# Kernel optimization log

Hardware: AMD Instinct MI355X
Metric: run time of the kernel (lower is better)

Reference implementation:

```python
import jax, jax.numpy as jnp
import numpy as np

B, H, L, N = 16, 128, 4096, 64
DT_MIN, DT_MAX = 0.001, 0.1


def _make_dplr_hippo(n):
    # NPLR HiPPO -> DPLR diagonalization (numpy, init-time only)
    p0 = np.sqrt(1 + 2 * np.arange(n))
    A = p0[:, None] * p0[None, :]
    A = -(np.tril(A) - np.diag(np.arange(n)))
    p = np.sqrt(np.arange(n) + 0.5)
    b = np.sqrt(2 * np.arange(n) + 1.0)
    S = A + p[:, None] * p[None, :]
    Lam_re = np.mean(np.diagonal(S)) * np.ones(n)
    Lam_im, V = np.linalg.eigh(S * -1j)
    p = V.conj().T @ p
    b = V.conj().T @ b
    return Lam_re + 1j * Lam_im, p, b


def setup_inputs() -> dict:
    key = jax.random.key(0)
    k1, k2, k3 = jax.random.split(key, 3)
    Lam, p, b = _make_dplr_hippo(N)
    tile = lambda a: jnp.tile(jnp.asarray(a, jnp.float32)[None], (H, 1))
    Lambda_re = tile(Lam.real)
    Lambda_im = tile(Lam.imag)
    P_ri = jnp.tile(jnp.stack([jnp.asarray(p.real, jnp.float32), jnp.asarray(p.imag, jnp.float32)], -1)[None], (H, 1, 1))
    B_ri = jnp.tile(jnp.stack([jnp.asarray(b.real, jnp.float32), jnp.asarray(b.imag, jnp.float32)], -1)[None], (H, 1, 1))
    C = (0.5 ** 0.5) * jax.random.normal(k1, (H, N, 2), jnp.float32)
    log_step = jax.random.uniform(k2, (H,)) * (np.log(DT_MAX) - np.log(DT_MIN)) + np.log(DT_MIN)
    D = jnp.ones((H,), jnp.float32)
    u = jax.random.normal(k3, (B, H, L), jnp.float32)
    return {"u": u, "Lambda_re": Lambda_re, "Lambda_im": Lambda_im, "P_ri": P_ri,
            "B_ri": B_ri, "C": C, "log_step": log_step.astype(jnp.float32), "D": D}


def reference(u, Lambda_re, Lambda_im, P_ri, B_ri, C, log_step, D):
    Lseq = u.shape[-1]
    # setup(): Lambda = clip(Lambda_re, max=-1e-4) + i*Lambda_im ; C complex ; step = exp(log_step)
    Lam = jnp.minimum(Lambda_re, -1e-4) + 1j * Lambda_im            # [H,N]
    P = P_ri[..., 0] + 1j * P_ri[..., 1]                             # [H,N]
    Bm = B_ri[..., 0] + 1j * B_ri[..., 1]                            # [H,N]
    Cc = C[..., 0] + 1j * C[..., 1]                                  # [H,N]
    step = jnp.exp(log_step)                                         # [H]
    # kernel_DPLR at the roots of unity
    Omega = jnp.exp(-2j * jnp.pi * (jnp.arange(Lseq) / Lseq))        # [L]
    g = (2.0 / step)[:, None] * ((1.0 - Omega) / (1.0 + Omega))[None, :]  # [H,L]
    c = 2.0 / (1.0 + Omega)                                          # [L]
    den = 1.0 / (g[:, :, None] - Lam[:, None, :])                    # [H,L,N] resolvent
    # four Cauchy dot products, batched: v stacked on last axis
    Vmat = jnp.stack([Cc.conj() * Bm, Cc.conj() * P, P.conj() * Bm, P.conj() * P], axis=-1)  # [H,N,4]
    Ks = jnp.einsum('hln,hnk->hlk', den, Vmat)                       # [H,L,4]
    k00, k01, k10, k11 = Ks[..., 0], Ks[..., 1], Ks[..., 2], Ks[..., 3]
    atRoots = c[None, :] * (k00 - k01 * (1.0 / (1.0 + k11)) * k10)   # [H,L]
    K = jnp.fft.ifft(atRoots, Lseq, axis=-1).real                    # [H,L] SSM kernel
    # causal FFT convolution: pad both to 2L
    ud = jnp.fft.rfft(jnp.pad(u, ((0, 0), (0, 0), (0, Lseq))), axis=-1)   # [B,H,L+1]
    Kd = jnp.fft.rfft(jnp.pad(K, ((0, 0), (0, Lseq))), axis=-1)           # [H,L+1]
    y = jnp.fft.irfft(ud * Kd[None], axis=-1)[..., :Lseq]            # [B,H,L]
    return y + D[None, :, None] * u
```

## Files before the change

### kernel.cpp

```cpp
#include <hip/hip_runtime.h>
#include <hip/hip_bf16.h>


#define PI_F 3.14159265358979323846f

__device__ __forceinline__ float2 cmulf(float2 a, float2 b) {
  return make_float2(a.x * b.x - a.y * b.y, a.x * b.y + a.y * b.x);
}
__device__ __forceinline__ void cmul_set(float2& v, float wr, float wi) {
  v = make_float2(v.x * wr - v.y * wi, v.x * wi + v.y * wr);
}
__device__ __forceinline__ int ad(int k) { return k + (k >> 4); }

template <int SIGN>
__device__ __forceinline__ void bfly4(float2& a, float2& b, float2& c,
                                      float2& d) {
  float t0x = a.x + c.x, t0y = a.y + c.y;
  float t1x = a.x - c.x, t1y = a.y - c.y;
  float t2x = b.x + d.x, t2y = b.y + d.y;
  float t3x = b.x - d.x, t3y = b.y - d.y;
  a = make_float2(t0x + t2x, t0y + t2y);
  c = make_float2(t0x - t2x, t0y - t2y);
  if (SIGN < 0) {
    b = make_float2(t1x + t3y, t1y - t3x);
    d = make_float2(t1x - t3y, t1y + t3x);
  } else {
    b = make_float2(t1x - t3y, t1y + t3x);
    d = make_float2(t1x + t3y, t1y - t3x);
  }
}

template <int SIGN>
__device__ __forceinline__ void fft16(float2 v[16]) {
  const float sg = (float)SIGN;
  const float C1 = 0.92387953251128674f;
  const float S1 = 0.38268343236508978f;
  const float R2 = 0.70710678118654752f;
  bfly4<SIGN>(v[0], v[4], v[8], v[12]);
  bfly4<SIGN>(v[1], v[5], v[9], v[13]);
  bfly4<SIGN>(v[2], v[6], v[10], v[14]);
  bfly4<SIGN>(v[3], v[7], v[11], v[15]);
  cmul_set(v[5], C1, sg * S1);
  cmul_set(v[6], R2, sg * R2);
  cmul_set(v[7], S1, sg * C1);
  cmul_set(v[9], R2, sg * R2);
  v[10] = make_float2(-sg * v[10].y, sg * v[10].x);
  cmul_set(v[11], -R2, sg * R2);
  cmul_set(v[13], S1, sg * C1);
  cmul_set(v[14], -R2, sg * R2);
  cmul_set(v[15], -C1, -sg * S1);
  float2 w[16];
#pragma unroll
  for (int g = 0; g < 4; ++g) {
    float2 x0 = v[4 * g], x1 = v[4 * g + 1], x2 = v[4 * g + 2],
           x3 = v[4 * g + 3];
    bfly4<SIGN>(x0, x1, x2, x3);
    w[g] = x0; w[g + 4] = x1; w[g + 8] = x2; w[g + 12] = x3;
  }
#pragma unroll
  for (int i = 0; i < 16; ++i) v[i] = w[i];
}

__device__ __forceinline__ void tw_apply(float2 v[16], float ang) {
  float sn, cn;
  __sincosf(ang, &sn, &cn);
  float2 w1 = make_float2(cn, sn), cw = w1;
#pragma unroll
  for (int g = 1; g < 16; ++g) {
    v[g] = cmulf(v[g], cw);
    if (g < 15) cw = cmulf(cw, w1);
  }
}

template <int SIGN>
__device__ void fft4096_regs(float2 v[16], float2* lds, int tid) {
  const int a = tid & 15, g2 = tid >> 4;
  fft16<SIGN>(v);
  tw_apply(v, (float)SIGN * (2.0f * PI_F / 4096.0f) * (float)tid);
  __syncthreads();
#pragma unroll
  for (int g = 0; g < 16; ++g) lds[tid * 17 + g] = v[g];
  __syncthreads();
#pragma unroll
  for (int b = 0; b < 16; ++b) v[b] = lds[a * 17 + b * 272 + g2];
  fft16<SIGN>(v);
  tw_apply(v, (float)SIGN * (2.0f * PI_F / 256.0f) * (float)a);
  __syncthreads();
#pragma unroll
  for (int b = 0; b < 16; ++b) lds[g2 * 17 + b * 273 + a] = v[b];
  __syncthreads();
#pragma unroll
  for (int a2 = 0; a2 < 16; ++a2) v[a2] = lds[g2 * 17 + a * 273 + a2];
  fft16<SIGN>(v);
}

template <int SIGN>
__device__ void fft4096_scr2nat(float2 v[16], float2* lds, int tid) {
  const int a = tid & 15, g2 = tid >> 4;
  fft16<SIGN>(v);
  __syncthreads();
#pragma unroll
  for (int r = 0; r < 16; ++r) lds[g2 * 17 + a * 273 + r] = v[r];
  __syncthreads();
#pragma unroll
  for (int b = 0; b < 16; ++b) v[b] = lds[g2 * 17 + b * 273 + a];
  tw_apply(v, (float)SIGN * (2.0f * PI_F / 256.0f) * (float)a);
  fft16<SIGN>(v);
  __syncthreads();
#pragma unroll
  for (int r = 0; r < 16; ++r) lds[272 * r + 17 * a + g2] = v[r];
  __syncthreads();
#pragma unroll
  for (int g = 0; g < 16; ++g) v[g] = lds[tid * 17 + g];
  tw_apply(v, (float)SIGN * (2.0f * PI_F / 4096.0f) * (float)tid);
  fft16<SIGN>(v);
}

__global__ __launch_bounds__(256) void k_cauchy(
    const float* __restrict__ Lre, const float* __restrict__ Lim,
    const float* __restrict__ Pri, const float* __restrict__ Bri,
    const float* __restrict__ Cri, const float* __restrict__ lstep,
    float2* __restrict__ atR) {
  __shared__ float4 pA[64];
  __shared__ float4 pB[64];
  __shared__ float2 pL[64];
  const int h = blockIdx.x >> 4;
  const int sub = blockIdx.x & 15;
  const int tid = threadIdx.x;
  if (tid < 64) {
    int base = h * 64 + tid;
    float lr = fminf(Lre[base], -1e-4f);
    float li = Lim[base];
    float pr = Pri[2 * base], pi = Pri[2 * base + 1];
    float br = Bri[2 * base], bi = Bri[2 * base + 1];
    float cr = Cri[2 * base], ci = Cri[2 * base + 1];
    pA[tid] = make_float4(cr * br + ci * bi, cr * bi - ci * br,
                          cr * pr + ci * pi, cr * pi - ci * pr);
    pB[tid] = make_float4(pr * br + pi * bi, pr * bi - pi * br,
                          pr * pr + pi * pi, 0.f);
    pL[tid] = make_float2(lr, li);
  }
  __syncthreads();
  const float istep = expf(-lstep[h]);
  const int m = sub * 256 + tid;
  float sn, cn;
  __sincosf(-(2.0f * PI_F / 4096.0f) * (float)m, &sn, &cn);
  const float trm = 0.5f * (1.0f + cn);
  const float tim = 0.5f * sn;
  const float qrm = (1.0f - cn) * istep;
  const float qim = -sn * istep;
  float S0 = 0.f, S1 = 0.f, S2 = 0.f, S3 = 0.f, S4 = 0.f, S5 = 0.f, S6 = 0.f,
        S7 = 0.f;
#pragma unroll 8
  for (int n = 0; n < 64; ++n) {
    float4 a = pA[n];
    float4 b = pB[n];
    float2 L = pL[n];
    float dr = qrm - (trm * L.x - tim * L.y);
    float di = qim - (trm * L.y + tim * L.x);
    float inv = __builtin_amdgcn_rcpf(dr * dr + di * di);
    float sr = dr * inv, si = -di * inv;
    S0 += a.x * sr - a.y * si;  S1 += a.x * si + a.y * sr;
    S2 += a.z * sr - a.w * si;  S3 += a.z * si + a.w * sr;
    S4 += b.x * sr - b.y * si;  S5 += b.x * si + b.y * sr;
    S6 += b.z * sr;             S7 += b.z * si;
  }
  float tS11r = trm * S6 - tim * S7;
  float tS11i = trm * S7 + tim * S6;
  float denr = 1.0f + tS11r, deni = tS11i;
  float dinv = 1.0f / (denr * denr + deni * deni);
  float P1r = S2 * S4 - S3 * S5;
  float P1i = S2 * S5 + S3 * S4;
  float P2r = trm * P1r - tim * P1i;
  float P2i = trm * P1i + tim * P1r;
  float Qr = (P2r * denr + P2i * deni) * dinv;
  float Qi = (P2i * denr - P2r * deni) * dinv;
  atR[h * 4096 + m] = make_float2(S0 - Qr, S1 - Qi);
}

__global__ __launch_bounds__(256, 4) void k_khat(
    const float2* __restrict__ atR, const float* __restrict__ Dp,
    float4* __restrict__ abt) {
  __shared__ float2 lds[4368];
  const int h = blockIdx.x;
  const int tid = threadIdx.x;
  float2 v[16];
#pragma unroll
  for (int c = 0; c < 16; ++c) v[c] = atR[h * 4096 + tid + 256 * c];
  fft4096_regs<1>(v, lds, tid);
  const int kb = (tid >> 4) + 16 * (tid & 15);
  float* ldsf = (float*)lds;
  const float s = 1.0f / 4096.0f;
  __syncthreads();
#pragma unroll
  for (int al = 0; al < 16; ++al) ldsf[ad(kb + 256 * al)] = v[al].x * s;
  __syncthreads();
#pragma unroll
  for (int c = 0; c < 8; ++c) {
    int n = tid + 256 * c;
    v[c] = make_float2(ldsf[ad(2 * n)], ldsf[ad(2 * n + 1)]);
  }
#pragma unroll
  for (int c = 8; c < 16; ++c) v[c] = make_float2(0.f, 0.f);
  fft4096_regs<-1>(v, lds, tid);
  __syncthreads();
#pragma unroll
  for (int al = 0; al < 16; ++al) lds[ad(kb + 256 * al)] = v[al];
  __syncthreads();
  const float Dh = Dp[h];
#pragma unroll
  for (int c = 0; c < 16; ++c) {
    int k = kb + 256 * c;
    float2 Zk = lds[ad(k)];
    float2 Zm = lds[ad((4096 - k) & 4095)];
    float Er = 0.5f * (Zk.x + Zm.x), Ei = 0.5f * (Zk.y - Zm.y);
    float Or = 0.5f * (Zk.y + Zm.y), Oi = 0.5f * (Zm.x - Zk.x);
    float s_, c_;
    __sincosf(-(PI_F / 4096.0f) * (float)k, &s_, &c_);
    float Gr = c_ * Or - s_ * Oi, Gi = c_ * Oi + s_ * Or;
    float ar = (Er + Dh + s_ * Gr) * s;
    float ai = (Ei + s_ * Gi) * s;
    float br = (-c_ * Gi) * s;
    float bi = (c_ * Gr) * s;
    abt[h * 4096 + tid + 256 * c] = make_float4(ar, ai, br, bi);
  }
}

__global__ __launch_bounds__(256, 4) void k_conv(const float* __restrict__ u,
                                                 const float4* __restrict__ abt,
                                                 float* __restrict__ y) {
  __shared__ float2 lds[4368];
  const int r = blockIdx.x;
  const int h = r & 127;
  const int tid = threadIdx.x;
  const float2* u2 = (const float2*)(u + (size_t)r * 4096);
  float2 v[16];
#pragma unroll
  for (int c = 0; c < 8; ++c) v[c] = u2[tid + 256 * c];
#pragma unroll
  for (int c = 8; c < 16; ++c) v[c] = make_float2(0.f, 0.f);
  fft4096_regs<-1>(v, lds, tid);
  const int kb = (tid >> 4) + 16 * (tid & 15);
  __syncthreads();
#pragma unroll
  for (int al = 0; al < 16; ++al) lds[ad(kb + 256 * al)] = v[al];
  __syncthreads();
  const float4* __restrict__ abrow = abt + h * 4096;
#pragma unroll
  for (int al = 0; al < 16; ++al) {
    int k = kb + 256 * al;
    float4 ab = abrow[tid + 256 * al];
    float2 Zm = lds[ad((4096 - k) & 4095)];
    float2 Zk = v[al];
    v[al] = make_float2(ab.x * Zk.x - ab.y * Zk.y + ab.z * Zm.x + ab.w * Zm.y,
                        ab.x * Zk.y + ab.y * Zk.x + ab.w * Zm.x - ab.z * Zm.y);
  }
  fft4096_scr2nat<1>(v, lds, tid);
  float2* y2 = (float2*)(y + (size_t)r * 4096);
#pragma unroll
  for (int c = 0; c < 8; ++c) y2[tid + 256 * c] = v[c];
}

extern "C" void kernel_launch(void* const* d_in, const int* in_sizes, int n_in,
                              void* d_out, int out_size, void* d_ws,
                              size_t ws_size, hipStream_t stream) {
  (void)in_sizes; (void)n_in; (void)out_size; (void)ws_size;
  const float* u = (const float*)d_in[0];
  const float* Lre = (const float*)d_in[1];
  const float* Lim = (const float*)d_in[2];
  const float* Pri = (const float*)d_in[3];
  const float* Bri = (const float*)d_in[4];
  const float* Cri = (const float*)d_in[5];
  const float* lst = (const float*)d_in[6];
  const float* Dp = (const float*)d_in[7];
  float* y = (float*)d_out;
  float2* atR = (float2*)d_ws;
  float4* abt = (float4*)((char*)d_ws + (size_t)4 * 1024 * 1024);

  k_cauchy<<<2048, 256, 0, stream>>>(Lre, Lim, Pri, Bri, Cri, lst, atR);
  k_khat<<<128, 256, 0, stream>>>(atR, Dp, abt);
  k_conv<<<2048, 256, 0, stream>>>(u, abt, y);
}
```

Baseline: 161.0 us.

## Rewrite convolution FFT as radix-8 with 512 threads per row

Replaces the 256-thread radix-16 three-pass 4096-point FFT in the convolution kernel with a 512-thread radix-8 four-pass FFT. The kernel-spectrum table is permuted into the new output digit order so the pointwise multiply needs no reordering. The aim is fewer registers per thread and more threads per row to hide latency. In exchange it adds an extra LDS transpose pass and more barriers in each direction.

```diff
diff --git a/kernel.cpp b/kernel.cpp
--- a/kernel.cpp
+++ b/kernel.cpp
@@ -11,6 +11,9 @@
   v = make_float2(v.x * wr - v.y * wi, v.x * wi + v.y * wr);
 }
 __device__ __forceinline__ int ad(int k) { return k + (k >> 4); }
+__device__ __forceinline__ int orev(int x) {
+  return ((x & 7) << 6) | (x & 56) | (x >> 6);
+}
 
 template <int SIGN>
 __device__ __forceinline__ void bfly4(float2& a, float2& b, float2& c,
@@ -28,6 +31,41 @@
     b = make_float2(t1x - t3y, t1y + t3x);
     d = make_float2(t1x + t3y, t1y - t3x);
   }
+}
+
+template <int SIGN>
+__device__ __forceinline__ void fft8(float2 v[8]) {
+  const float sg = (float)SIGN;
+  const float R2 = 0.70710678118654752f;
+  float2 e0 = make_float2(v[0].x + v[4].x, v[0].y + v[4].y);
+  float2 o0 = make_float2(v[0].x - v[4].x, v[0].y - v[4].y);
+  float2 e1 = make_float2(v[1].x + v[5].x, v[1].y + v[5].y);
+  float2 o1 = make_float2(v[1].x - v[5].x, v[1].y - v[5].y);
+  float2 e2 = make_float2(v[2].x + v[6].x, v[2].y + v[6].y);
+  float2 o2 = make_float2(v[2].x - v[6].x, v[2].y - v[6].y);
+  float2 e3 = make_float2(v[3].x + v[7].x, v[3].y + v[7].y);
+  float2 o3 = make_float2(v[3].x - v[7].x, v[3].y - v[7].y);
+  cmul_set(o1, R2, sg * R2);
+  o2 = make_float2(-sg * o2.y, sg * o2.x);
+  cmul_set(o3, -R2, sg * R2);
+  bfly4<SIGN>(e0, e1, e2, e3);
+  bfly4<SIGN>(o0, o1, o2, o3);
+  v[0] = e0; v[1] = o0; v[2] = e1; v[3] = o1;
+  v[4] = e2; v[5] = o2; v[6] = e3; v[7] = o3;
+}
+
+__device__ __forceinline__ void tw8(float2 v[8], float c, float s) {
+  float2 p1 = make_float2(c, s);
+  float2 p2 = cmulf(p1, p1);
+  float2 p3 = cmulf(p1, p2);
+  float2 p4 = cmulf(p2, p2);
+  float2 p5 = cmulf(p2, p3);
+  float2 p6 = cmulf(p3, p3);
+  float2 p7 = cmulf(p3, p4);
+  v[1] = cmulf(v[1], p1); v[2] = cmulf(v[2], p2);
+  v[3] = cmulf(v[3], p3); v[4] = cmulf(v[4], p4);
+  v[5] = cmulf(v[5], p5); v[6] = cmulf(v[6], p6);
+  v[7] = cmulf(v[7], p7);
 }
 
 template <int SIGN>
@@ -91,28 +129,6 @@
   __syncthreads();
 #pragma unroll
   for (int a2 = 0; a2 < 16; ++a2) v[a2] = lds[g2 * 17 + a * 273 + a2];
-  fft16<SIGN>(v);
-}
-
-template <int SIGN>
-__device__ void fft4096_scr2nat(float2 v[16], float2* lds, int tid) {
-  const int a = tid & 15, g2 = tid >> 4;
-  fft16<SIGN>(v);
-  __syncthreads();
-#pragma unroll
-  for (int r = 0; r < 16; ++r) lds[g2 * 17 + a * 273 + r] = v[r];
-  __syncthreads();
-#pragma unroll
-  for (int b = 0; b < 16; ++b) v[b] = lds[g2 * 17 + b * 273 + a];
-  tw_apply(v, (float)SIGN * (2.0f * PI_F / 256.0f) * (float)a);
-  fft16<SIGN>(v);
-  __syncthreads();
-#pragma unroll
-  for (int r = 0; r < 16; ++r) lds[272 * r + 17 * a + g2] = v[r];
-  __syncthreads();
-#pragma unroll
-  for (int g = 0; g < 16; ++g) v[g] = lds[tid * 17 + g];
-  tw_apply(v, (float)SIGN * (2.0f * PI_F / 4096.0f) * (float)tid);
   fft16<SIGN>(v);
 }
 
@@ -222,43 +238,99 @@
     float ai = (Ei + s_ * Gi) * s;
     float br = (-c_ * Gi) * s;
     float bi = (c_ * Gr) * s;
-    abt[h * 4096 + tid + 256 * c] = make_float4(ar, ai, br, bi);
-  }
-}
-
-__global__ __launch_bounds__(256, 4) void k_conv(const float* __restrict__ u,
-                                                 const float4* __restrict__ abt,
-                                                 float* __restrict__ y) {
-  __shared__ float2 lds[4368];
+    int slot = orev(k & 511) + ((k >> 9) << 9);
+    abt[h * 4096 + slot] = make_float4(ar, ai, br, bi);
+  }
+}
+
+__global__ __launch_bounds__(512, 4) void k_conv8(
+    const float* __restrict__ u, const float4* __restrict__ abt,
+    float* __restrict__ y) {
+  __shared__ float2 lds[4712];
   const int r = blockIdx.x;
   const int h = r & 127;
-  const int tid = threadIdx.x;
+  const int t = threadIdx.x;
+  const int t0 = t & 7, t1 = (t >> 3) & 7, t2 = t >> 6;
+  float c_t, s_t, c_6, s_6, c_0, s_0;
+  __sincosf((2.0f * PI_F / 4096.0f) * (float)t, &s_t, &c_t);
+  __sincosf((2.0f * PI_F / 512.0f) * (float)(t & 63), &s_6, &c_6);
+  __sincosf((2.0f * PI_F / 64.0f) * (float)t0, &s_0, &c_0);
+
   const float2* u2 = (const float2*)(u + (size_t)r * 4096);
-  float2 v[16];
-#pragma unroll
-  for (int c = 0; c < 8; ++c) v[c] = u2[tid + 256 * c];
-#pragma unroll
-  for (int c = 8; c < 16; ++c) v[c] = make_float2(0.f, 0.f);
-  fft4096_regs<-1>(v, lds, tid);
-  const int kb = (tid >> 4) + 16 * (tid & 15);
-  __syncthreads();
-#pragma unroll
-  for (int al = 0; al < 16; ++al) lds[ad(kb + 256 * al)] = v[al];
-  __syncthreads();
+  float2 v[8];
+#pragma unroll
+  for (int c = 0; c < 4; ++c) v[c] = u2[t + 512 * c];
+#pragma unroll
+  for (int c = 4; c < 8; ++c) v[c] = make_float2(0.f, 0.f);
+
+  fft8<-1>(v);
+  tw8(v, c_t, -s_t);
+#pragma unroll
+  for (int g = 0; g < 8; ++g) lds[589 * g + 74 * t0 + 9 * t1 + t2] = v[g];
+  __syncthreads();
+#pragma unroll
+  for (int b = 0; b < 8; ++b) v[b] = lds[589 * t2 + 74 * t0 + 9 * t1 + b];
+  fft8<-1>(v);
+  tw8(v, c_6, -s_6);
+  __syncthreads();
+#pragma unroll
+  for (int g = 0; g < 8; ++g) lds[589 * t2 + 74 * t0 + 9 * t1 + g] = v[g];
+  __syncthreads();
+#pragma unroll
+  for (int b = 0; b < 8; ++b) v[b] = lds[589 * t2 + 74 * t0 + 9 * b + t1];
+  fft8<-1>(v);
+  tw8(v, c_0, -s_0);
+  __syncthreads();
+#pragma unroll
+  for (int g = 0; g < 8; ++g) lds[589 * t2 + 74 * t1 + 9 * t0 + g] = v[g];
+  __syncthreads();
+#pragma unroll
+  for (int b = 0; b < 8; ++b) v[b] = lds[589 * t2 + 74 * t1 + 9 * b + t0];
+  fft8<-1>(v);
+  __syncthreads();
+#pragma unroll
+  for (int g = 0; g < 8; ++g) lds[t + 512 * g] = v[g];
+  __syncthreads();
+  const int kb = orev(t);
   const float4* __restrict__ abrow = abt + h * 4096;
 #pragma unroll
-  for (int al = 0; al < 16; ++al) {
-    int k = kb + 256 * al;
-    float4 ab = abrow[tid + 256 * al];
-    float2 Zm = lds[ad((4096 - k) & 4095)];
-    float2 Zk = v[al];
-    v[al] = make_float2(ab.x * Zk.x - ab.y * Zk.y + ab.z * Zm.x + ab.w * Zm.y,
-                        ab.x * Zk.y + ab.y * Zk.x + ab.w * Zm.x - ab.z * Zm.y);
-  }
-  fft4096_scr2nat<1>(v, lds, tid);
+  for (int g = 0; g < 8; ++g) {
+    int k = kb + 512 * g;
+    int kp = (4096 - k) & 4095;
+    float2 Zm = lds[orev(kp & 511) + ((kp >> 9) << 9)];
+    float4 ab = abrow[t + 512 * g];
+    float2 Zk = v[g];
+    v[g] = make_float2(ab.x * Zk.x - ab.y * Zk.y + ab.z * Zm.x + ab.w * Zm.y,
+                       ab.x * Zk.y + ab.y * Zk.x + ab.w * Zm.x - ab.z * Zm.y);
+  }
+  fft8<1>(v);
+  __syncthreads();
+#pragma unroll
+  for (int g = 0; g < 8; ++g) lds[589 * t2 + 74 * t1 + 9 * g + t0] = v[g];
+  __syncthreads();
+#pragma unroll
+  for (int b = 0; b < 8; ++b) v[b] = lds[589 * t2 + 74 * t1 + 9 * t0 + b];
+  tw8(v, c_0, s_0);
+  fft8<1>(v);
+  __syncthreads();
+#pragma unroll
+  for (int g = 0; g < 8; ++g) lds[589 * t2 + 74 * t0 + 9 * g + t1] = v[g];
+  __syncthreads();
+#pragma unroll
+  for (int b = 0; b < 8; ++b) v[b] = lds[589 * t2 + 74 * t0 + 9 * t1 + b];
+  tw8(v, c_6, s_6);
+  fft8<1>(v);
+  __syncthreads();
+#pragma unroll
+  for (int g = 0; g < 8; ++g) lds[589 * t2 + 74 * t0 + 9 * t1 + g] = v[g];
+  __syncthreads();
+#pragma unroll
+  for (int b = 0; b < 8; ++b) v[b] = lds[589 * b + 74 * t0 + 9 * t1 + t2];
+  tw8(v, c_t, s_t);
+  fft8<1>(v);
   float2* y2 = (float2*)(y + (size_t)r * 4096);
 #pragma unroll
-  for (int c = 0; c < 8; ++c) y2[tid + 256 * c] = v[c];
+  for (int c = 0; c < 4; ++c) y2[t + 512 * c] = v[c];
 }
 
 extern "C" void kernel_launch(void* const* d_in, const int* in_sizes, int n_in,
@@ -279,5 +351,5 @@
 
   k_cauchy<<<2048, 256, 0, stream>>>(Lre, Lim, Pri, Bri, Cri, lst, atR);
   k_khat<<<128, 256, 0, stream>>>(atR, Dp, abt);
-  k_conv<<<2048, 256, 0, stream>>>(u, abt, y);
-}
+  k_conv8<<<2048, 512, 0, stream>>>(u, abt, y);
+}
```

After: 160.3 us. Within noise of the previous version (-0.4%).
